# Kernel optimization log

Hardware: AMD Instinct MI355X
Metric: run time of the kernel (lower is better)

## Reference

```python
import jax, jax.numpy as jnp
import numpy as np

N_OSC = 32
CONV = 1000.0  # convergence_factor


def _cpg_ode(y, ia, ifr, cw, pb):
    # Faithful to CPGOde.forward, including its unpacking order:
    # (amplitudes, amplitudes_dot, phases) = (y[:n], y[n:2n], y[2n:3n])
    n = N_OSC
    a = y[:n]
    a_dot = y[n:2 * n]
    ph = y[2 * n:3 * n]
    phase_dots = ifr + jnp.sum(a[:, None] * cw * jnp.sin(ph[None, :] - ph[:, None] - pb), axis=1)
    a_dd = CONV * (CONV / 4.0 * (ia - a) - a_dot)
    # states_to_tensor(amplitudes_dot, phase_dots, amplitudes_dot_dot)
    return jnp.concatenate([a_dot, phase_dots, a_dd])


def _rk4_38_step(f, y, h):
    # torchdiffeq 'rk4' = rk4_alt_step_func (3/8 rule), one step over t=[0, h]
    k1 = f(y)
    k2 = f(y + h * k1 / 3.0)
    k3 = f(y + h * (k2 - k1 / 3.0))
    k4 = f(y + h * (k1 - k2 + k3))
    return y + h * 0.125 * (k1 + 3.0 * (k2 + k3) + k4)


def _mlp(x, Ws, bs):
    # Linear stack with ReLU between layers, none after the last
    for i, (W, b) in enumerate(zip(Ws, bs)):
        x = W @ x + b
        if i < len(Ws) - 1:
            x = jax.nn.relu(x)
    return x


def _init_linear(key, fan_in, fan_out):
    kW, kb = jax.random.split(key)
    bound = 1.0 / np.sqrt(fan_in)
    W = jax.random.uniform(kW, (fan_out, fan_in), minval=-bound, maxval=bound, dtype=jnp.float32)
    b = jax.random.uniform(kb, (fan_out,), minval=-bound, maxval=bound, dtype=jnp.float32)
    return W, b


def setup_inputs() -> dict:
    key = jax.random.key(0)
    ks = jax.random.split(key, 10)
    n = N_OSC
    n_params = 2 * n + 2 * n * n  # 2112
    in_dims = [2049, 4096, 4096, n_params]  # input_layers[0]+1, ..., final param layer
    out_dims = [2 * n, 2048, 2048, 1024]
    inp = {}
    inp["state"] = jax.random.normal(ks[0], (3 * n,), dtype=jnp.float32) * 0.1
    inp["x"] = jax.random.normal(ks[1], (2048,), dtype=jnp.float32)
    inp["timestep"] = jnp.array(0.01, dtype=jnp.float32)
    for i in range(3):
        W, b = _init_linear(ks[2 + i], in_dims[i], in_dims[i + 1])
        inp[f"in_W{i}"] = W
        inp[f"in_b{i}"] = b
    for i in range(3):
        W, b = _init_linear(ks[5 + i], out_dims[i], out_dims[i + 1])
        inp[f"out_W{i}"] = W
        inp[f"out_b{i}"] = b
    return inp


def reference(state, x, timestep,
              in_W0, in_b0, in_W1, in_b1, in_W2, in_b2,
              out_W0, out_b0, out_W1, out_b1, out_W2, out_b2):
    n = N_OSC
    # append timestep scalar to the input features
    x = jnp.concatenate([x, timestep[None]])
    params = _mlp(x, [in_W0, in_W1, in_W2], [in_b0, in_b1, in_b2])
    ia = params[:n]
    ifr = params[n:2 * n]
    cw = params[2 * n:2 * n + n * n].reshape(n, n)
    pb = params[2 * n + n * n:].reshape(n, n)
    f = lambda y: _cpg_ode(y, ia, ifr, cw, pb)
    new_state = _rk4_38_step(f, state, timestep)
    a = new_state[:n]
    ph = new_state[n:2 * n]
    cpg_out = jnp.concatenate([a * jnp.cos(ph), a * jnp.sin(ph)])
    out = _mlp(cpg_out, [out_W0, out_W1, out_W2], [out_b0, out_b1, out_b2])
    return (jax.lax.stop_gradient(new_state), out)
```

## Files before the change

### kernel.cpp

```cpp
#include <hip/hip_runtime.h>
#include <stdint.h>

template<int RELU, int TSCOL>
__global__ __launch_bounds__(256, 4) void gemv_k(
    const float* __restrict__ W, const float* __restrict__ B,
    const float* __restrict__ x, const float* __restrict__ ts,
    float* __restrict__ y, int rows, int cols)
{
    int wv   = threadIdx.x >> 6;
    int lane = threadIdx.x & 63;
    int row  = blockIdx.x * 4 + wv;
    if (row >= rows) return;

    int n = TSCOL ? cols - 1 : cols;
    const float* w = W + (size_t)row * (size_t)cols;
    float sum = 0.0f;

    int mis = (int)(((uintptr_t)w >> 2) & 3);
    int start = (4 - mis) & 3;
    if (start > n) start = n;
    if (lane < start) sum += w[lane] * x[lane];
    int nv = (n - start) >> 2;
    const float4* wp = (const float4*)(w + start);
    const float* xs = x + start;
    int g = lane;
    for (; g + 448 < nv; g += 512) {
        float4 u0 = wp[g];
        float4 u1 = wp[g + 64];
        float4 u2 = wp[g + 128];
        float4 u3 = wp[g + 192];
        float4 u4 = wp[g + 256];
        float4 u5 = wp[g + 320];
        float4 u6 = wp[g + 384];
        float4 u7 = wp[g + 448];
        const float* x0 = xs + 4 * g;
        sum += u0.x * x0[0]    + u0.y * x0[1]    + u0.z * x0[2]    + u0.w * x0[3];
        sum += u1.x * x0[256]  + u1.y * x0[257]  + u1.z * x0[258]  + u1.w * x0[259];
        sum += u2.x * x0[512]  + u2.y * x0[513]  + u2.z * x0[514]  + u2.w * x0[515];
        sum += u3.x * x0[768]  + u3.y * x0[769]  + u3.z * x0[770]  + u3.w * x0[771];
        sum += u4.x * x0[1024] + u4.y * x0[1025] + u4.z * x0[1026] + u4.w * x0[1027];
        sum += u5.x * x0[1280] + u5.y * x0[1281] + u5.z * x0[1282] + u5.w * x0[1283];
        sum += u6.x * x0[1536] + u6.y * x0[1537] + u6.z * x0[1538] + u6.w * x0[1539];
        sum += u7.x * x0[1792] + u7.y * x0[1793] + u7.z * x0[1794] + u7.w * x0[1795];
    }
    for (; g < nv; g += 64) {
        float4 u = wp[g];
        const float* xp = xs + 4 * g;
        sum += u.x * xp[0] + u.y * xp[1] + u.z * xp[2] + u.w * xp[3];
    }
    int t = start + nv * 4 + lane;
    if (t < n) sum += w[t] * x[t];
    if (TSCOL && lane == 0) sum += w[n] * ts[0];

    #pragma unroll
    for (int off = 32; off > 0; off >>= 1) sum += __shfl_down(sum, off);

    if (lane == 0) {
        float r = sum + B[row];
        if (RELU) r = fmaxf(r, 0.0f);
        y[row] = r;
    }
}

template<int RELU>
__global__ __launch_bounds__(256, 4) void gemv1_k(
    const float* __restrict__ W, const float* __restrict__ B,
    const float* __restrict__ x, float* __restrict__ y, int cols)
{
    int row  = blockIdx.x * 4 + (threadIdx.x >> 6);
    int lane = threadIdx.x & 63;

    const float4* wp = (const float4*)(W + (size_t)row * (size_t)cols);
    const float4* xp = (const float4*)x;
    int nv = cols >> 2;

    float s = 0.0f;
    int g = lane;
    for (; g + 448 < nv; g += 512) {
        float4 xv0 = xp[g];       float4 a0 = wp[g];
        float4 xv1 = xp[g + 64];  float4 a1 = wp[g + 64];
        float4 xv2 = xp[g + 128]; float4 a2 = wp[g + 128];
        float4 xv3 = xp[g + 192]; float4 a3 = wp[g + 192];
        float4 xv4 = xp[g + 256]; float4 a4 = wp[g + 256];
        float4 xv5 = xp[g + 320]; float4 a5 = wp[g + 320];
        float4 xv6 = xp[g + 384]; float4 a6 = wp[g + 384];
        float4 xv7 = xp[g + 448]; float4 a7 = wp[g + 448];
        s += a0.x*xv0.x + a0.y*xv0.y + a0.z*xv0.z + a0.w*xv0.w;
        s += a1.x*xv1.x + a1.y*xv1.y + a1.z*xv1.z + a1.w*xv1.w;
        s += a2.x*xv2.x + a2.y*xv2.y + a2.z*xv2.z + a2.w*xv2.w;
        s += a3.x*xv3.x + a3.y*xv3.y + a3.z*xv3.z + a3.w*xv3.w;
        s += a4.x*xv4.x + a4.y*xv4.y + a4.z*xv4.z + a4.w*xv4.w;
        s += a5.x*xv5.x + a5.y*xv5.y + a5.z*xv5.z + a5.w*xv5.w;
        s += a6.x*xv6.x + a6.y*xv6.y + a6.z*xv6.z + a6.w*xv6.w;
        s += a7.x*xv7.x + a7.y*xv7.y + a7.z*xv7.z + a7.w*xv7.w;
    }
    for (; g < nv; g += 64) {
        float4 xv = xp[g];
        float4 a = wp[g];
        s += a.x*xv.x + a.y*xv.y + a.z*xv.z + a.w*xv.w;
    }

    #pragma unroll
    for (int off = 32; off > 0; off >>= 1) s += __shfl_down(s, off);

    if (lane == 0) {
        float v = s + B[row];
        if (RELU) v = fmaxf(v, 0.0f);
        y[row] = v;
    }
}

__global__ __launch_bounds__(256) void ode_ow0_k(
    const float* __restrict__ state, const float* __restrict__ ts,
    const float* __restrict__ params,
    const float* __restrict__ oW0, const float* __restrict__ ob0,
    float* __restrict__ g0, float* __restrict__ out_state)
{
    const float CONV = 1000.0f;
    __shared__ float s_cw[32 * 33];
    __shared__ float s_spb[32 * 33];
    __shared__ float s_cpb[32 * 33];
    __shared__ float s_s[32], s_c[32];
    __shared__ float s_cpg[64];
    int tid = threadIdx.x;

    for (int k = tid; k < 1024; k += 256) {
        int p = k + (k >> 5);
        s_cw[p] = params[64 + k];
        float sp, cp;
        sincosf(params[1088 + k], &sp, &cp);
        s_spb[p] = sp;
        s_cpb[p] = cp;
    }
    __syncthreads();

    bool act = (tid < 32);
    int i = tid;
    float ia = 0.f, ifr = 0.f, y0a = 0.f, y0b = 0.f, y0c = 0.f;
    if (act) {
        ia  = params[i];
        ifr = params[32 + i];
        y0a = state[i];
        y0b = state[32 + i];
        y0c = state[64 + i];
    }
    float h = ts[0];

    float k1a=0,k1b=0,k1c=0, k2a=0,k2b=0,k2c=0, k3a=0,k3b=0,k3c=0, k4a=0,k4b=0,k4c=0;

    auto do_eval = [&](float a, float ad, float ph,
                       float& fa, float& fb, float& fc) {
        __syncthreads();
        if (act) {
            float s, c;
            sincosf(ph, &s, &c);
            s_s[i] = s; s_c[i] = c;
        }
        __syncthreads();
        if (act) {
            float si = s_s[i], ci = s_c[i];
            float ssum = 0.0f;
            #pragma unroll
            for (int j = 0; j < 32; j++) {
                float sj = s_s[j], cj = s_c[j];
                float sdp = sj * ci - cj * si;
                float cdp = cj * ci + sj * si;
                int p = i * 33 + j;
                float sv = sdp * s_cpb[p] - cdp * s_spb[p];
                ssum += s_cw[p] * sv;
            }
            fa = ad;
            fb = ifr + a * ssum;
            fc = CONV * (CONV * 0.25f * (ia - a) - ad);
        }
    };

    do_eval(y0a, y0b, y0c, k1a, k1b, k1c);
    do_eval(y0a + h * k1a / 3.0f,
            y0b + h * k1b / 3.0f,
            y0c + h * k1c / 3.0f, k2a, k2b, k2c);
    do_eval(y0a + h * (k2a - k1a / 3.0f),
            y0b + h * (k2b - k1b / 3.0f),
            y0c + h * (k2c - k1c / 3.0f), k3a, k3b, k3c);
    do_eval(y0a + h * (k1a - k2a + k3a),
            y0b + h * (k1b - k2b + k3b),
            y0c + h * (k1c - k2c + k3c), k4a, k4b, k4c);

    if (act) {
        float na = y0a + h * 0.125f * (k1a + 3.0f * (k2a + k3a) + k4a);
        float nb = y0b + h * 0.125f * (k1b + 3.0f * (k2b + k3b) + k4b);
        float nc = y0c + h * 0.125f * (k1c + 3.0f * (k2c + k3c) + k4c);
        if (blockIdx.x == 0) {
            out_state[i]      = na;
            out_state[32 + i] = nb;
            out_state[64 + i] = nc;
        }
        s_cpg[i]      = na * cosf(nb);
        s_cpg[32 + i] = na * sinf(nb);
    }
    __syncthreads();

    int wv   = tid >> 6;
    int lane = tid & 63;
    int row  = blockIdx.x * 4 + wv;
    float sum = oW0[(size_t)row * 64 + lane] * s_cpg[lane];
    #pragma unroll
    for (int off = 32; off > 0; off >>= 1) sum += __shfl_down(sum, off);
    if (lane == 0) g0[row] = fmaxf(sum + ob0[row], 0.0f);
}

extern "C" void kernel_launch(void* const* d_in, const int* in_sizes, int n_in,
                              void* d_out, int out_size, void* d_ws, size_t ws_size,
                              hipStream_t stream) {
    const float* state = (const float*)d_in[0];
    const float* x     = (const float*)d_in[1];
    const float* ts    = (const float*)d_in[2];
    const float* inW0  = (const float*)d_in[3];
    const float* inb0  = (const float*)d_in[4];
    const float* inW1  = (const float*)d_in[5];
    const float* inb1  = (const float*)d_in[6];
    const float* inW2  = (const float*)d_in[7];
    const float* inb2  = (const float*)d_in[8];
    const float* oW0   = (const float*)d_in[9];
    const float* ob0   = (const float*)d_in[10];
    const float* oW1   = (const float*)d_in[11];
    const float* ob1   = (const float*)d_in[12];
    const float* oW2   = (const float*)d_in[13];
    const float* ob2   = (const float*)d_in[14];

    float* ws  = (float*)d_ws;
    float* h0  = ws;
    float* h1  = ws + 4096;
    float* pr  = ws + 8192;
    float* g0  = ws + 10368;
    float* g1  = ws + 12416;

    float* out = (float*)d_out;

    gemv_k<1,1><<<1024, 256, 0, stream>>>(inW0, inb0, x, ts, h0, 4096, 2049);
    gemv1_k<1><<<1024, 256, 0, stream>>>(inW1, inb1, h0, h1, 4096);
    gemv1_k<0><<<528,  256, 0, stream>>>(inW2, inb2, h1, pr, 4096);
    ode_ow0_k<<<512, 256, 0, stream>>>(state, ts, pr, oW0, ob0, g0, out);
    gemv1_k<1><<<512,  256, 0, stream>>>(oW1, ob1, g0, g1, 2048);
    gemv1_k<0><<<256,  256, 0, stream>>>(oW2, ob2, g1, out + 96, 2048);
}
```

Baseline: 215.6 us.

## Fuse all MLP and ODE stages into one persistent kernel with grid barriers

Replaces the six separate launches (three input GEMVs, the fused ODE plus first output layer, and two output GEMVs) with one persistent kernel of 512 blocks × 512 threads. Stages are separated by an atomic-counter grid barrier that is reset with a memset, and intermediates are written with agent-scope atomic stores. The goal is to remove launch gaps and the tail idle time between dependent stages. The trade-offs are barrier spin cost and load imbalance, since some stages use only half or a quarter of the waves. It also relies on all blocks being co-resident and on cross-XCD visibility of plain loads after relaxed atomics. The GEMV inner loops are unrolled 4 deep instead of 8.

```diff
diff --git a/kernel.cpp b/kernel.cpp
--- a/kernel.cpp
+++ b/kernel.cpp
@@ -1,120 +1,67 @@
 #include <hip/hip_runtime.h>
 #include <stdint.h>
 
-template<int RELU, int TSCOL>
-__global__ __launch_bounds__(256, 4) void gemv_k(
-    const float* __restrict__ W, const float* __restrict__ B,
-    const float* __restrict__ x, const float* __restrict__ ts,
-    float* __restrict__ y, int rows, int cols)
-{
-    int wv   = threadIdx.x >> 6;
-    int lane = threadIdx.x & 63;
-    int row  = blockIdx.x * 4 + wv;
-    if (row >= rows) return;
-
-    int n = TSCOL ? cols - 1 : cols;
-    const float* w = W + (size_t)row * (size_t)cols;
-    float sum = 0.0f;
-
-    int mis = (int)(((uintptr_t)w >> 2) & 3);
-    int start = (4 - mis) & 3;
-    if (start > n) start = n;
-    if (lane < start) sum += w[lane] * x[lane];
-    int nv = (n - start) >> 2;
-    const float4* wp = (const float4*)(w + start);
-    const float* xs = x + start;
-    int g = lane;
-    for (; g + 448 < nv; g += 512) {
-        float4 u0 = wp[g];
-        float4 u1 = wp[g + 64];
-        float4 u2 = wp[g + 128];
-        float4 u3 = wp[g + 192];
-        float4 u4 = wp[g + 256];
-        float4 u5 = wp[g + 320];
-        float4 u6 = wp[g + 384];
-        float4 u7 = wp[g + 448];
-        const float* x0 = xs + 4 * g;
-        sum += u0.x * x0[0]    + u0.y * x0[1]    + u0.z * x0[2]    + u0.w * x0[3];
-        sum += u1.x * x0[256]  + u1.y * x0[257]  + u1.z * x0[258]  + u1.w * x0[259];
-        sum += u2.x * x0[512]  + u2.y * x0[513]  + u2.z * x0[514]  + u2.w * x0[515];
-        sum += u3.x * x0[768]  + u3.y * x0[769]  + u3.z * x0[770]  + u3.w * x0[771];
-        sum += u4.x * x0[1024] + u4.y * x0[1025] + u4.z * x0[1026] + u4.w * x0[1027];
-        sum += u5.x * x0[1280] + u5.y * x0[1281] + u5.z * x0[1282] + u5.w * x0[1283];
-        sum += u6.x * x0[1536] + u6.y * x0[1537] + u6.z * x0[1538] + u6.w * x0[1539];
-        sum += u7.x * x0[1792] + u7.y * x0[1793] + u7.z * x0[1794] + u7.w * x0[1795];
-    }
-    for (; g < nv; g += 64) {
-        float4 u = wp[g];
-        const float* xp = xs + 4 * g;
-        sum += u.x * xp[0] + u.y * xp[1] + u.z * xp[2] + u.w * xp[3];
-    }
-    int t = start + nv * 4 + lane;
-    if (t < n) sum += w[t] * x[t];
-    if (TSCOL && lane == 0) sum += w[n] * ts[0];
-
+#define NBLK 512
+#define NTHR 512
+
+__device__ __forceinline__ float wave_reduce(float s) {
     #pragma unroll
-    for (int off = 32; off > 0; off >>= 1) sum += __shfl_down(sum, off);
-
-    if (lane == 0) {
-        float r = sum + B[row];
-        if (RELU) r = fmaxf(r, 0.0f);
-        y[row] = r;
-    }
-}
-
-template<int RELU>
-__global__ __launch_bounds__(256, 4) void gemv1_k(
-    const float* __restrict__ W, const float* __restrict__ B,
-    const float* __restrict__ x, float* __restrict__ y, int cols)
-{
-    int row  = blockIdx.x * 4 + (threadIdx.x >> 6);
-    int lane = threadIdx.x & 63;
-
-    const float4* wp = (const float4*)(W + (size_t)row * (size_t)cols);
-    const float4* xp = (const float4*)x;
+    for (int off = 32; off > 0; off >>= 1) s += __shfl_down(s, off);
+    return s;
+}
+
+__device__ __forceinline__ float dot_row_aligned(const float* __restrict__ w,
+                                                 const float* __restrict__ xv,
+                                                 int cols, int lane) {
+    const float4* wp = (const float4*)w;
+    const float4* xp = (const float4*)xv;
     int nv = cols >> 2;
-
     float s = 0.0f;
     int g = lane;
-    for (; g + 448 < nv; g += 512) {
-        float4 xv0 = xp[g];       float4 a0 = wp[g];
-        float4 xv1 = xp[g + 64];  float4 a1 = wp[g + 64];
-        float4 xv2 = xp[g + 128]; float4 a2 = wp[g + 128];
-        float4 xv3 = xp[g + 192]; float4 a3 = wp[g + 192];
-        float4 xv4 = xp[g + 256]; float4 a4 = wp[g + 256];
-        float4 xv5 = xp[g + 320]; float4 a5 = wp[g + 320];
-        float4 xv6 = xp[g + 384]; float4 a6 = wp[g + 384];
-        float4 xv7 = xp[g + 448]; float4 a7 = wp[g + 448];
-        s += a0.x*xv0.x + a0.y*xv0.y + a0.z*xv0.z + a0.w*xv0.w;
-        s += a1.x*xv1.x + a1.y*xv1.y + a1.z*xv1.z + a1.w*xv1.w;
-        s += a2.x*xv2.x + a2.y*xv2.y + a2.z*xv2.z + a2.w*xv2.w;
-        s += a3.x*xv3.x + a3.y*xv3.y + a3.z*xv3.z + a3.w*xv3.w;
-        s += a4.x*xv4.x + a4.y*xv4.y + a4.z*xv4.z + a4.w*xv4.w;
-        s += a5.x*xv5.x + a5.y*xv5.y + a5.z*xv5.z + a5.w*xv5.w;
-        s += a6.x*xv6.x + a6.y*xv6.y + a6.z*xv6.z + a6.w*xv6.w;
-        s += a7.x*xv7.x + a7.y*xv7.y + a7.z*xv7.z + a7.w*xv7.w;
+    for (; g + 192 < nv; g += 256) {
+        float4 x0 = xp[g];       float4 a0 = wp[g];
+        float4 x1 = xp[g + 64];  float4 a1 = wp[g + 64];
+        float4 x2 = xp[g + 128]; float4 a2 = wp[g + 128];
+        float4 x3 = xp[g + 192]; float4 a3 = wp[g + 192];
+        s += a0.x*x0.x + a0.y*x0.y + a0.z*x0.z + a0.w*x0.w;
+        s += a1.x*x1.x + a1.y*x1.y + a1.z*x1.z + a1.w*x1.w;
+        s += a2.x*x2.x + a2.y*x2.y + a2.z*x2.z + a2.w*x2.w;
+        s += a3.x*x3.x + a3.y*x3.y + a3.z*x3.z + a3.w*x3.w;
     }
     for (; g < nv; g += 64) {
-        float4 xv = xp[g];
-        float4 a = wp[g];
-        s += a.x*xv.x + a.y*xv.y + a.z*xv.z + a.w*xv.w;
-    }
-
-    #pragma unroll
-    for (int off = 32; off > 0; off >>= 1) s += __shfl_down(s, off);
-
-    if (lane == 0) {
-        float v = s + B[row];
-        if (RELU) v = fmaxf(v, 0.0f);
-        y[row] = v;
-    }
-}
-
-__global__ __launch_bounds__(256) void ode_ow0_k(
-    const float* __restrict__ state, const float* __restrict__ ts,
-    const float* __restrict__ params,
+        float4 xq = xp[g]; float4 a = wp[g];
+        s += a.x*xq.x + a.y*xq.y + a.z*xq.z + a.w*xq.w;
+    }
+    return s;
+}
+
+__device__ __forceinline__ void st_agent(float* p, float v) {
+    __hip_atomic_store(p, v, __ATOMIC_RELAXED, __HIP_MEMORY_SCOPE_AGENT);
+}
+
+__device__ __forceinline__ void gbar(int* __restrict__ bar, int k) {
+    __syncthreads();
+    if (threadIdx.x == 0) {
+        __hip_atomic_fetch_add(&bar[k], 1, __ATOMIC_RELAXED, __HIP_MEMORY_SCOPE_AGENT);
+        while (__hip_atomic_load(&bar[k], __ATOMIC_RELAXED, __HIP_MEMORY_SCOPE_AGENT) < NBLK) {
+            __builtin_amdgcn_s_sleep(4);
+        }
+    }
+    __syncthreads();
+}
+
+__global__ __launch_bounds__(NTHR, 4) void fused_k(
+    const float* __restrict__ state, const float* __restrict__ x,
+    const float* __restrict__ ts,
+    const float* __restrict__ inW0, const float* __restrict__ inb0,
+    const float* __restrict__ inW1, const float* __restrict__ inb1,
+    const float* __restrict__ inW2, const float* __restrict__ inb2,
     const float* __restrict__ oW0, const float* __restrict__ ob0,
-    float* __restrict__ g0, float* __restrict__ out_state)
+    const float* __restrict__ oW1, const float* __restrict__ ob1,
+    const float* __restrict__ oW2, const float* __restrict__ ob2,
+    float* __restrict__ h0, float* __restrict__ h1, float* __restrict__ pr,
+    float* __restrict__ g0, float* __restrict__ g1, float* __restrict__ out,
+    int* __restrict__ bar)
 {
     const float CONV = 1000.0f;
     __shared__ float s_cw[32 * 33];
@@ -122,91 +69,165 @@
     __shared__ float s_cpb[32 * 33];
     __shared__ float s_s[32], s_c[32];
     __shared__ float s_cpg[64];
-    int tid = threadIdx.x;
-
-    for (int k = tid; k < 1024; k += 256) {
+
+    int tid  = threadIdx.x;
+    int lane = tid & 63;
+    int gw   = blockIdx.x * 8 + (tid >> 6);
+
+    {
+        const float* w = inW0 + (size_t)gw * 2049;
+        const int n = 2048;
+        float sum = 0.0f;
+        int mis = (int)(((uintptr_t)w >> 2) & 3);
+        int start = (4 - mis) & 3;
+        if (lane < start) sum += w[lane] * x[lane];
+        int nv = (n - start) >> 2;
+        const float4* wp = (const float4*)(w + start);
+        const float* xs = x + start;
+        int g = lane;
+        for (; g + 192 < nv; g += 256) {
+            float4 u0 = wp[g];
+            float4 u1 = wp[g + 64];
+            float4 u2 = wp[g + 128];
+            float4 u3 = wp[g + 192];
+            const float* x0 = xs + 4 * g;
+            sum += u0.x * x0[0]   + u0.y * x0[1]   + u0.z * x0[2]   + u0.w * x0[3];
+            sum += u1.x * x0[256] + u1.y * x0[257] + u1.z * x0[258] + u1.w * x0[259];
+            sum += u2.x * x0[512] + u2.y * x0[513] + u2.z * x0[514] + u2.w * x0[515];
+            sum += u3.x * x0[768] + u3.y * x0[769] + u3.z * x0[770] + u3.w * x0[771];
+        }
+        for (; g < nv; g += 64) {
+            float4 u = wp[g];
+            const float* xp2 = xs + 4 * g;
+            sum += u.x * xp2[0] + u.y * xp2[1] + u.z * xp2[2] + u.w * xp2[3];
+        }
+        int t = start + nv * 4 + lane;
+        if (t < n) sum += w[t] * x[t];
+        if (lane == 0) sum += w[n] * ts[0];
+        sum = wave_reduce(sum);
+        if (lane == 0) st_agent(&h0[gw], fmaxf(sum + inb0[gw], 0.0f));
+    }
+    gbar(bar, 0);
+
+    {
+        float s = dot_row_aligned(inW1 + (size_t)gw * 4096, h0, 4096, lane);
+        s = wave_reduce(s);
+        if (lane == 0) st_agent(&h1[gw], fmaxf(s + inb1[gw], 0.0f));
+    }
+    gbar(bar, 1);
+
+    {
+        int r3 = -1;
+        if ((gw & 1) == 0) r3 = gw >> 1;
+        else { int q = gw >> 1; if (q >= 1984) r3 = 2048 + (q - 1984); }
+        if (r3 >= 0) {
+            float s = dot_row_aligned(inW2 + (size_t)r3 * 4096, h1, 4096, lane);
+            s = wave_reduce(s);
+            if (lane == 0) st_agent(&pr[r3], s + inb2[r3]);
+        }
+    }
+    gbar(bar, 2);
+
+    for (int k = tid; k < 1024; k += NTHR) {
         int p = k + (k >> 5);
-        s_cw[p] = params[64 + k];
+        s_cw[p] = pr[64 + k];
         float sp, cp;
-        sincosf(params[1088 + k], &sp, &cp);
+        sincosf(pr[1088 + k], &sp, &cp);
         s_spb[p] = sp;
         s_cpb[p] = cp;
     }
     __syncthreads();
 
-    bool act = (tid < 32);
-    int i = tid;
-    float ia = 0.f, ifr = 0.f, y0a = 0.f, y0b = 0.f, y0c = 0.f;
-    if (act) {
-        ia  = params[i];
-        ifr = params[32 + i];
-        y0a = state[i];
-        y0b = state[32 + i];
-        y0c = state[64 + i];
-    }
-    float h = ts[0];
-
-    float k1a=0,k1b=0,k1c=0, k2a=0,k2b=0,k2c=0, k3a=0,k3b=0,k3c=0, k4a=0,k4b=0,k4c=0;
-
-    auto do_eval = [&](float a, float ad, float ph,
-                       float& fa, float& fb, float& fc) {
-        __syncthreads();
+    {
+        bool act = (tid < 32);
+        int i = tid;
+        float ia = 0.f, ifr = 0.f, y0a = 0.f, y0b = 0.f, y0c = 0.f;
         if (act) {
-            float s, c;
-            sincosf(ph, &s, &c);
-            s_s[i] = s; s_c[i] = c;
-        }
-        __syncthreads();
+            ia  = pr[i];
+            ifr = pr[32 + i];
+            y0a = state[i];
+            y0b = state[32 + i];
+            y0c = state[64 + i];
+        }
+        float h = ts[0];
+
+        float k1a=0,k1b=0,k1c=0, k2a=0,k2b=0,k2c=0, k3a=0,k3b=0,k3c=0, k4a=0,k4b=0,k4c=0;
+
+        auto do_eval = [&](float a, float ad, float ph,
+                           float& fa, float& fb, float& fc) {
+            __syncthreads();
+            if (act) {
+                float s, c;
+                sincosf(ph, &s, &c);
+                s_s[i] = s; s_c[i] = c;
+            }
+            __syncthreads();
+            if (act) {
+                float si = s_s[i], ci = s_c[i];
+                float ssum = 0.0f;
+                #pragma unroll
+                for (int j = 0; j < 32; j++) {
+                    float sj = s_s[j], cj = s_c[j];
+                    float sdp = sj * ci - cj * si;
+                    float cdp = cj * ci + sj * si;
+                    int p = i * 33 + j;
+                    float sv = sdp * s_cpb[p] - cdp * s_spb[p];
+                    ssum += s_cw[p] * sv;
+                }
+                fa = ad;
+                fb = ifr + a * ssum;
+                fc = CONV * (CONV * 0.25f * (ia - a) - ad);
+            }
+        };
+
+        do_eval(y0a, y0b, y0c, k1a, k1b, k1c);
+        do_eval(y0a + h * k1a / 3.0f,
+                y0b + h * k1b / 3.0f,
+                y0c + h * k1c / 3.0f, k2a, k2b, k2c);
+        do_eval(y0a + h * (k2a - k1a / 3.0f),
+                y0b + h * (k2b - k1b / 3.0f),
+                y0c + h * (k2c - k1c / 3.0f), k3a, k3b, k3c);
+        do_eval(y0a + h * (k1a - k2a + k3a),
+                y0b + h * (k1b - k2b + k3b),
+                y0c + h * (k1c - k2c + k3c), k4a, k4b, k4c);
+
         if (act) {
-            float si = s_s[i], ci = s_c[i];
-            float ssum = 0.0f;
-            #pragma unroll
-            for (int j = 0; j < 32; j++) {
-                float sj = s_s[j], cj = s_c[j];
-                float sdp = sj * ci - cj * si;
-                float cdp = cj * ci + sj * si;
-                int p = i * 33 + j;
-                float sv = sdp * s_cpb[p] - cdp * s_spb[p];
-                ssum += s_cw[p] * sv;
+            float na = y0a + h * 0.125f * (k1a + 3.0f * (k2a + k3a) + k4a);
+            float nb = y0b + h * 0.125f * (k1b + 3.0f * (k2b + k3b) + k4b);
+            float nc = y0c + h * 0.125f * (k1c + 3.0f * (k2c + k3c) + k4c);
+            if (blockIdx.x == 0) {
+                out[i]      = na;
+                out[32 + i] = nb;
+                out[64 + i] = nc;
             }
-            fa = ad;
-            fb = ifr + a * ssum;
-            fc = CONV * (CONV * 0.25f * (ia - a) - ad);
-        }
-    };
-
-    do_eval(y0a, y0b, y0c, k1a, k1b, k1c);
-    do_eval(y0a + h * k1a / 3.0f,
-            y0b + h * k1b / 3.0f,
-            y0c + h * k1c / 3.0f, k2a, k2b, k2c);
-    do_eval(y0a + h * (k2a - k1a / 3.0f),
-            y0b + h * (k2b - k1b / 3.0f),
-            y0c + h * (k2c - k1c / 3.0f), k3a, k3b, k3c);
-    do_eval(y0a + h * (k1a - k2a + k3a),
-            y0b + h * (k1b - k2b + k3b),
-            y0c + h * (k1c - k2c + k3c), k4a, k4b, k4c);
-
-    if (act) {
-        float na = y0a + h * 0.125f * (k1a + 3.0f * (k2a + k3a) + k4a);
-        float nb = y0b + h * 0.125f * (k1b + 3.0f * (k2b + k3b) + k4b);
-        float nc = y0c + h * 0.125f * (k1c + 3.0f * (k2c + k3c) + k4c);
-        if (blockIdx.x == 0) {
-            out_state[i]      = na;
-            out_state[32 + i] = nb;
-            out_state[64 + i] = nc;
-        }
-        s_cpg[i]      = na * cosf(nb);
-        s_cpg[32 + i] = na * sinf(nb);
-    }
-    __syncthreads();
-
-    int wv   = tid >> 6;
-    int lane = tid & 63;
-    int row  = blockIdx.x * 4 + wv;
-    float sum = oW0[(size_t)row * 64 + lane] * s_cpg[lane];
-    #pragma unroll
-    for (int off = 32; off > 0; off >>= 1) sum += __shfl_down(sum, off);
-    if (lane == 0) g0[row] = fmaxf(sum + ob0[row], 0.0f);
+            s_cpg[i]      = na * cosf(nb);
+            s_cpg[32 + i] = na * sinf(nb);
+        }
+    }
+    __syncthreads();
+
+    if ((gw & 1) == 0) {
+        int r = gw >> 1;
+        float sum = oW0[(size_t)r * 64 + lane] * s_cpg[lane];
+        sum = wave_reduce(sum);
+        if (lane == 0) st_agent(&g0[r], fmaxf(sum + ob0[r], 0.0f));
+    }
+    gbar(bar, 3);
+
+    if ((gw & 1) == 0) {
+        int r = gw >> 1;
+        float s = dot_row_aligned(oW1 + (size_t)r * 2048, g0, 2048, lane);
+        s = wave_reduce(s);
+        if (lane == 0) st_agent(&g1[r], fmaxf(s + ob1[r], 0.0f));
+    }
+    gbar(bar, 4);
+
+    if ((gw & 3) == 0) {
+        int r = gw >> 2;
+        float s = dot_row_aligned(oW2 + (size_t)r * 2048, g1, 2048, lane);
+        s = wave_reduce(s);
+        if (lane == 0) out[96 + r] = s + ob2[r];
+    }
 }
 
 extern "C" void kernel_launch(void* const* d_in, const int* in_sizes, int n_in,
@@ -234,13 +255,15 @@
     float* pr  = ws + 8192;
     float* g0  = ws + 10368;
     float* g1  = ws + 12416;
+    int*   bar = (int*)(ws + 24576);
 
     float* out = (float*)d_out;
 
-    gemv_k<1,1><<<1024, 256, 0, stream>>>(inW0, inb0, x, ts, h0, 4096, 2049);
-    gemv1_k<1><<<1024, 256, 0, stream>>>(inW1, inb1, h0, h1, 4096);
-    gemv1_k<0><<<528,  256, 0, stream>>>(inW2, inb2, h1, pr, 4096);
-    ode_ow0_k<<<512, 256, 0, stream>>>(state, ts, pr, oW0, ob0, g0, out);
-    gemv1_k<1><<<512,  256, 0, stream>>>(oW1, ob1, g0, g1, 2048);
-    gemv1_k<0><<<256,  256, 0, stream>>>(oW2, ob2, g1, out + 96, 2048);
-}
+    hipMemsetAsync(bar, 0, 64, stream);
+
+    fused_k<<<NBLK, NTHR, 0, stream>>>(
+        state, x, ts,
+        inW0, inb0, inW1, inb1, inW2, inb2,
+        oW0, ob0, oW1, ob1, oW2, ob2,
+        h0, h1, pr, g0, g1, out, bar);
+}
```

After: 293.5 us. 36.1% more time.
